# Kernel optimization log

Hardware: AMD Instinct MI355X
Metric: run time of the kernel (lower is better)

## Reference

```python
import jax, jax.numpy as jnp
import numpy as np


def setup_inputs() -> dict:
    key = jax.random.key(0)
    kq, kk, kv = jax.random.split(key, 3)
    B, S, H, D = 2, 2048, 16, 64
    q = jax.random.normal(kq, (B, S, H, D), dtype=jnp.float32)
    k = jax.random.normal(kk, (B, S, H, D), dtype=jnp.float32)
    v = jax.random.normal(kv, (B, S, H, D), dtype=jnp.float32)
    # additive key padding mask, [B,1,1,K]; 0 = unmasked, -inf = masked
    key_padding_mask = jnp.zeros((B, 1, 1, S), dtype=jnp.float32)
    return {"q": q, "k": k, "v": v, "key_padding_mask": key_padding_mask}


def reference(q, k, v, key_padding_mask):
    # q,k,v: [B, S, H, D]; key_padding_mask: [B,1,1,K] additive
    head_dim = q.shape[-1]
    softmax_scale = 1.0 / np.sqrt(head_dim).astype(np.float32)
    # [B, H, Q, K] logits with additive mask
    logits = jnp.einsum('bqhd,bkhd->bhqk', q, k) * softmax_scale + key_padding_mask
    attn = jax.nn.softmax(logits, axis=-1)
    # dropout p=0.0 -> identity in eval mode
    out = jnp.einsum('bhqk,bkhd->bqhd', attn, v)
    return out
```

## Files before the change

kernel.cpp:

```cpp
#include <hip/hip_runtime.h>
#include <hip/hip_bf16.h>


typedef __attribute__((ext_vector_type(8))) short bf16x8;
typedef __attribute__((ext_vector_type(4))) short bf16x4;
typedef __attribute__((ext_vector_type(4))) float f32x4;

#define B_ 2
#define S_ 2048
#define H_ 16
#define D_ 64
#define BQ 128
#define BK 64
#define NT (S_ / BK)
#define ROWSZ (H_ * D_)

#define LOG2E  1.44269504088896340736f
#define SCALE2 (0.125f * LOG2E)

__device__ __forceinline__ unsigned pack2(float a, float b) {
    union { __hip_bfloat162 h; unsigned u; } x;
    x.h = __float22bfloat162_rn(make_float2(a, b));
    return x.u;
}

__device__ __forceinline__ float fexp2(float x) {
#if __has_builtin(__builtin_amdgcn_exp2f)
    return __builtin_amdgcn_exp2f(x);
#else
    return __expf(x * 0.69314718055994531f);
#endif
}

__device__ __forceinline__ f32x4 mfma16(bf16x4 a, bf16x4 b, f32x4 c) {
#if __has_builtin(__builtin_amdgcn_mfma_f32_16x16x16bf16_1k)
    return __builtin_amdgcn_mfma_f32_16x16x16bf16_1k(a, b, c, 0, 0, 0);
#else
    bf16x8 a8 = {a[0], a[1], a[2], a[3], 0, 0, 0, 0};
    bf16x8 b8 = {b[0], b[1], b[2], b[3], 0, 0, 0, 0};
    return __builtin_amdgcn_mfma_f32_16x16x32_bf16(a8, b8, c, 0, 0, 0);
#endif
}

__global__ __launch_bounds__(512, 4)
void fattn_kernel(const float* __restrict__ qg,
                  const float* __restrict__ kg,
                  const float* __restrict__ vg,
                  const float* __restrict__ maskg,
                  float* __restrict__ outg)
{
    __shared__ __attribute__((aligned(16))) ushort Ks[2][4096];
    __shared__ __attribute__((aligned(16))) ushort Vt[2][4096];
    __shared__ __attribute__((aligned(16))) float  Em[S_];

    const int qt = blockIdx.x, h = blockIdx.y, b = blockIdx.z;
    const int tid = threadIdx.x;
    const int w = tid >> 6, lane = tid & 63, g = lane >> 4, l15 = lane & 15;

    {
        float4 mv = *(const float4*)(maskg + (size_t)b * S_ + tid * 4);
        *(float4*)&Em[tid * 4] = make_float4(mv.x * LOG2E, mv.y * LOG2E,
                                             mv.z * LOG2E, mv.w * LOG2E);
    }

    const int qrow = qt * BQ + w * 16 + l15;
    const float* qp = qg + (size_t)(b * S_ + qrow) * ROWSZ + h * D_;
    bf16x8 qf[2];
#pragma unroll
    for (int half = 0; half < 2; ++half) {
        float4 f0 = *(const float4*)(qp + half * 32 + g * 8);
        float4 f1 = *(const float4*)(qp + half * 32 + g * 8 + 4);
        union { bf16x8 v; uint4 u; } x;
        x.u = make_uint4(pack2(f0.x * SCALE2, f0.y * SCALE2),
                         pack2(f0.z * SCALE2, f0.w * SCALE2),
                         pack2(f1.x * SCALE2, f1.y * SCALE2),
                         pack2(f1.z * SCALE2, f1.w * SCALE2));
        qf[half] = x.v;
    }

    const int skey = tid >> 4;
    const int sd   = (tid & 15) * 4;
    const int kw0 = (skey >> 4) * 1024
                  + ((sd >> 3) + ((skey >> 3) & 1) * 8) * 64
                  + (((skey & 7) ^ (sd >> 3)) << 3) + (sd & 7);
    const int kw1 = kw0 + 2048;
    const int vwA = ((w >> 1) * 4 + (lane >> 4)) * 256
                  + ((2 * w) & 3) * 64 + (lane & 15) * 4;
    const int vwB = vwA + 64;

    const size_t kvbase = (size_t)b * S_ * ROWSZ + h * D_;

    float4 kpre0, kpre1;
    float  vpre[8];
    auto prefetch = [&](int kt) {
        const float* kb = kg + kvbase + (size_t)kt * BK * ROWSZ;
        kpre0 = *(const float4*)(kb + (size_t)skey * ROWSZ + sd);
        kpre1 = *(const float4*)(kb + (size_t)(skey + 32) * ROWSZ + sd);
        const float* vb = vg + kvbase + (size_t)kt * BK * ROWSZ + lane;
#pragma unroll
        for (int i = 0; i < 8; ++i) vpre[i] = vb[(size_t)(w * 8 + i) * ROWSZ];
    };
    auto stage = [&](int buf) {
        *(uint2*)&Ks[buf][kw0] =
            make_uint2(pack2(kpre0.x, kpre0.y), pack2(kpre0.z, kpre0.w));
        *(uint2*)&Ks[buf][kw1] =
            make_uint2(pack2(kpre1.x, kpre1.y), pack2(kpre1.z, kpre1.w));
        *(uint2*)&Vt[buf][vwA] =
            make_uint2(pack2(vpre[0], vpre[1]), pack2(vpre[2], vpre[3]));
        *(uint2*)&Vt[buf][vwB] =
            make_uint2(pack2(vpre[4], vpre[5]), pack2(vpre[6], vpre[7]));
    };

    float l_r = 0.0f;
    f32x4 o_acc[4];
#pragma unroll
    for (int t = 0; t < 4; ++t) o_acc[t] = (f32x4){0.f, 0.f, 0.f, 0.f};

    prefetch(0);
    stage(0);
    __syncthreads();

    const int krd0 = (g + (l15 >> 3) * 8) * 64 + (((l15 & 7) ^ g) << 3);
    const int krd1 = (g + 4 + (l15 >> 3) * 8) * 64 + (((l15 & 7) ^ (g + 4)) << 3);
    const int vrd = g * 64 + l15 * 4;

    for (int kt = 0; kt < NT; ++kt) {
        const int cur = kt & 1;
        if (kt + 1 < NT) prefetch(kt + 1);

        const ushort* ks = Ks[cur];
        float sv[4][4];
#pragma unroll
        for (int t = 0; t < 4; ++t) {
            f32x4 acc = *(const f32x4*)&Em[kt * BK + t * 16 + g * 4];
            bf16x8 kf0 = *(const bf16x8*)&ks[t * 1024 + krd0];
            bf16x8 kf1 = *(const bf16x8*)&ks[t * 1024 + krd1];
            acc = __builtin_amdgcn_mfma_f32_16x16x32_bf16(kf0, qf[0], acc, 0, 0, 0);
            acc = __builtin_amdgcn_mfma_f32_16x16x32_bf16(kf1, qf[1], acc, 0, 0, 0);
            sv[t][0] = acc[0]; sv[t][1] = acc[1]; sv[t][2] = acc[2]; sv[t][3] = acc[3];
        }

        float rs = 0.f;
#pragma unroll
        for (int t = 0; t < 4; ++t)
#pragma unroll
            for (int r = 0; r < 4; ++r) {
                float p = fexp2(sv[t][r]);
                sv[t][r] = p;
                rs += p;
            }
        l_r += rs;

        bf16x4 pf[4];
#pragma unroll
        for (int c = 0; c < 4; ++c) {
            union { bf16x4 v; uint2 u; } x;
            x.u = make_uint2(pack2(sv[c][0], sv[c][1]), pack2(sv[c][2], sv[c][3]));
            pf[c] = x.v;
        }

        const ushort* vt = Vt[cur];
#pragma unroll
        for (int c = 0; c < 4; ++c)
#pragma unroll
            for (int t2 = 0; t2 < 4; ++t2) {
                bf16x4 vf = *(const bf16x4*)&vt[(c * 4 + t2) * 256 + vrd];
                o_acc[t2] = mfma16(vf, pf[c], o_acc[t2]);
            }

        if (kt + 1 < NT) stage(cur ^ 1);
        __syncthreads();
    }

    l_r += __shfl_xor(l_r, 16);
    l_r += __shfl_xor(l_r, 32);
    const float inv = 1.0f / l_r;
    float* op = outg + (size_t)(b * S_ + qrow) * ROWSZ + h * D_;
#pragma unroll
    for (int t2 = 0; t2 < 4; ++t2)
#pragma unroll
        for (int r = 0; r < 4; ++r)
            op[t2 * 16 + g * 4 + r] = o_acc[t2][r] * inv;
}

extern "C" void kernel_launch(void* const* d_in, const int* in_sizes, int n_in,
                              void* d_out, int out_size, void* d_ws, size_t ws_size,
                              hipStream_t stream) {
    dim3 grid(S_ / BQ, H_, B_);
    fattn_kernel<<<grid, dim3(512), 0, stream>>>(
        (const float*)d_in[0], (const float*)d_in[1], (const float*)d_in[2],
        (const float*)d_in[3], (float*)d_out);
}
```

Baseline: 144.9 us.

## Split key sequence across two blocks and combine partial attention outputs

The attention kernel now splits the key/value sequence into two halves, each handled by its own block. Each block writes unnormalized partial outputs and row sums to workspace, and a second combine kernel adds them and normalizes. The goal is to double the number of blocks, raise occupancy and give the GPU more parallelism on a grid that was only 512 blocks. The exp/pack step is also folded into the QK loop. The cost is an extra kernel launch and substantial workspace write and read traffic; the original kernel is kept as a fallback when no workspace is provided.

New measurement: 170.2 us. 17.5% more time.

```diff
diff --git a/kernel.cpp b/kernel.cpp
--- a/kernel.cpp
+++ b/kernel.cpp
@@ -12,8 +12,13 @@
 #define D_ 64
 #define BQ 128
 #define BK 64
+#define QT_ (S_ / BQ)
+#define NSP 2
 #define NT (S_ / BK)
+#define NTH (NT / NSP)
 #define ROWSZ (H_ * D_)
+#define NREG (B_ * H_ * QT_ * NSP)
+#define REGSZ (512 * 16)
 
 #define LOG2E  1.44269504088896340736f
 #define SCALE2 (0.125f * LOG2E)
@@ -42,23 +47,26 @@
 #endif
 }
 
-__global__ __launch_bounds__(512, 4)
-void fattn_kernel(const float* __restrict__ qg,
-                  const float* __restrict__ kg,
-                  const float* __restrict__ vg,
-                  const float* __restrict__ maskg,
-                  float* __restrict__ outg)
+__global__ __launch_bounds__(512, 8)
+void fattn_split(const float* __restrict__ qg,
+                 const float* __restrict__ kg,
+                 const float* __restrict__ vg,
+                 const float* __restrict__ maskg,
+                 float* __restrict__ wso,
+                 float* __restrict__ wsl)
 {
     __shared__ __attribute__((aligned(16))) ushort Ks[2][4096];
     __shared__ __attribute__((aligned(16))) ushort Vt[2][4096];
-    __shared__ __attribute__((aligned(16))) float  Em[S_];
-
-    const int qt = blockIdx.x, h = blockIdx.y, b = blockIdx.z;
+    __shared__ __attribute__((aligned(16))) float  Em[S_ / NSP];
+
+    const int qt = blockIdx.x & 15, sp = blockIdx.x >> 4;
+    const int h = blockIdx.y, b = blockIdx.z;
     const int tid = threadIdx.x;
     const int w = tid >> 6, lane = tid & 63, g = lane >> 4, l15 = lane & 15;
 
-    {
-        float4 mv = *(const float4*)(maskg + (size_t)b * S_ + tid * 4);
+    if (tid < 256) {
+        float4 mv = *(const float4*)(maskg + (size_t)b * S_
+                                     + sp * (S_ / NSP) + tid * 4);
         *(float4*)&Em[tid * 4] = make_float4(mv.x * LOG2E, mv.y * LOG2E,
                                              mv.z * LOG2E, mv.w * LOG2E);
     }
@@ -88,15 +96,18 @@
                   + ((2 * w) & 3) * 64 + (lane & 15) * 4;
     const int vwB = vwA + 64;
 
-    const size_t kvbase = (size_t)b * S_ * ROWSZ + h * D_;
+    const size_t kvbase = (size_t)b * S_ * ROWSZ + h * D_
+                        + (size_t)sp * (S_ / NSP) * ROWSZ;
+    const float* kgs = kg + kvbase;
+    const float* vgs = vg + kvbase;
 
     float4 kpre0, kpre1;
     float  vpre[8];
-    auto prefetch = [&](int kt) {
-        const float* kb = kg + kvbase + (size_t)kt * BK * ROWSZ;
+    auto prefetch = [&](int ktl) {
+        const float* kb = kgs + (size_t)ktl * BK * ROWSZ;
         kpre0 = *(const float4*)(kb + (size_t)skey * ROWSZ + sd);
         kpre1 = *(const float4*)(kb + (size_t)(skey + 32) * ROWSZ + sd);
-        const float* vb = vg + kvbase + (size_t)kt * BK * ROWSZ + lane;
+        const float* vb = vgs + (size_t)ktl * BK * ROWSZ + lane;
 #pragma unroll
         for (int i = 0; i < 8; ++i) vpre[i] = vb[(size_t)(w * 8 + i) * ROWSZ];
     };
@@ -124,6 +135,162 @@
     const int krd1 = (g + 4 + (l15 >> 3) * 8) * 64 + (((l15 & 7) ^ (g + 4)) << 3);
     const int vrd = g * 64 + l15 * 4;
 
+    for (int ktl = 0; ktl < NTH; ++ktl) {
+        const int cur = ktl & 1;
+        if (ktl + 1 < NTH) prefetch(ktl + 1);
+
+        const ushort* ks = Ks[cur];
+        bf16x4 pf[4];
+        float rs = 0.f;
+#pragma unroll
+        for (int t = 0; t < 4; ++t) {
+            f32x4 acc = *(const f32x4*)&Em[ktl * BK + t * 16 + g * 4];
+            bf16x8 kf0 = *(const bf16x8*)&ks[t * 1024 + krd0];
+            bf16x8 kf1 = *(const bf16x8*)&ks[t * 1024 + krd1];
+            acc = __builtin_amdgcn_mfma_f32_16x16x32_bf16(kf0, qf[0], acc, 0, 0, 0);
+            acc = __builtin_amdgcn_mfma_f32_16x16x32_bf16(kf1, qf[1], acc, 0, 0, 0);
+            float p0 = fexp2(acc[0]), p1 = fexp2(acc[1]);
+            float p2 = fexp2(acc[2]), p3 = fexp2(acc[3]);
+            rs += (p0 + p1) + (p2 + p3);
+            union { bf16x4 v; uint2 u; } x;
+            x.u = make_uint2(pack2(p0, p1), pack2(p2, p3));
+            pf[t] = x.v;
+        }
+        l_r += rs;
+
+        const ushort* vt = Vt[cur];
+#pragma unroll
+        for (int c = 0; c < 4; ++c)
+#pragma unroll
+            for (int t2 = 0; t2 < 4; ++t2) {
+                bf16x4 vf = *(const bf16x4*)&vt[(c * 4 + t2) * 256 + vrd];
+                o_acc[t2] = mfma16(vf, pf[c], o_acc[t2]);
+            }
+
+        if (ktl + 1 < NTH) stage(cur ^ 1);
+        __syncthreads();
+    }
+
+    l_r += __shfl_xor(l_r, 16);
+    l_r += __shfl_xor(l_r, 32);
+
+    const int region = ((b * H_ + h) * QT_ + qt) * NSP + sp;
+    float* po = wso + (size_t)region * REGSZ + tid * 16;
+#pragma unroll
+    for (int t2 = 0; t2 < 4; ++t2) *(f32x4*)(po + t2 * 4) = o_acc[t2];
+    wsl[(size_t)region * 512 + tid] = l_r;
+}
+
+__global__ __launch_bounds__(512, 8)
+void fattn_combine(const float* __restrict__ wso,
+                   const float* __restrict__ wsl,
+                   float* __restrict__ outg)
+{
+    const int qt = blockIdx.x, h = blockIdx.y, b = blockIdx.z;
+    const int tid = threadIdx.x;
+    const int w = tid >> 6, lane = tid & 63, g = lane >> 4, l15 = lane & 15;
+
+    const int bhq = (b * H_ + h) * QT_ + qt;
+    const float* p0 = wso + (size_t)(bhq * NSP + 0) * REGSZ + tid * 16;
+    const float* p1 = wso + (size_t)(bhq * NSP + 1) * REGSZ + tid * 16;
+    const float  l  = wsl[(size_t)(bhq * NSP + 0) * 512 + tid]
+                    + wsl[(size_t)(bhq * NSP + 1) * 512 + tid];
+    const float inv = 1.0f / l;
+
+    const int qrow = qt * BQ + w * 16 + l15;
+    float* op = outg + (size_t)(b * S_ + qrow) * ROWSZ + h * D_;
+#pragma unroll
+    for (int t2 = 0; t2 < 4; ++t2) {
+        f32x4 a = *(const f32x4*)(p0 + t2 * 4);
+        f32x4 c = *(const f32x4*)(p1 + t2 * 4);
+#pragma unroll
+        for (int r = 0; r < 4; ++r)
+            op[t2 * 16 + g * 4 + r] = (a[r] + c[r]) * inv;
+    }
+}
+
+__global__ __launch_bounds__(512, 4)
+void fattn_kernel(const float* __restrict__ qg,
+                  const float* __restrict__ kg,
+                  const float* __restrict__ vg,
+                  const float* __restrict__ maskg,
+                  float* __restrict__ outg)
+{
+    __shared__ __attribute__((aligned(16))) ushort Ks[2][4096];
+    __shared__ __attribute__((aligned(16))) ushort Vt[2][4096];
+    __shared__ __attribute__((aligned(16))) float  Em[S_];
+
+    const int qt = blockIdx.x, h = blockIdx.y, b = blockIdx.z;
+    const int tid = threadIdx.x;
+    const int w = tid >> 6, lane = tid & 63, g = lane >> 4, l15 = lane & 15;
+
+    {
+        float4 mv = *(const float4*)(maskg + (size_t)b * S_ + tid * 4);
+        *(float4*)&Em[tid * 4] = make_float4(mv.x * LOG2E, mv.y * LOG2E,
+                                             mv.z * LOG2E, mv.w * LOG2E);
+    }
+
+    const int qrow = qt * BQ + w * 16 + l15;
+    const float* qp = qg + (size_t)(b * S_ + qrow) * ROWSZ + h * D_;
+    bf16x8 qf[2];
+#pragma unroll
+    for (int half = 0; half < 2; ++half) {
+        float4 f0 = *(const float4*)(qp + half * 32 + g * 8);
+        float4 f1 = *(const float4*)(qp + half * 32 + g * 8 + 4);
+        union { bf16x8 v; uint4 u; } x;
+        x.u = make_uint4(pack2(f0.x * SCALE2, f0.y * SCALE2),
+                         pack2(f0.z * SCALE2, f0.w * SCALE2),
+                         pack2(f1.x * SCALE2, f1.y * SCALE2),
+                         pack2(f1.z * SCALE2, f1.w * SCALE2));
+        qf[half] = x.v;
+    }
+
+    const int skey = tid >> 4;
+    const int sd   = (tid & 15) * 4;
+    const int kw0 = (skey >> 4) * 1024
+                  + ((sd >> 3) + ((skey >> 3) & 1) * 8) * 64
+                  + (((skey & 7) ^ (sd >> 3)) << 3) + (sd & 7);
+    const int kw1 = kw0 + 2048;
+    const int vwA = ((w >> 1) * 4 + (lane >> 4)) * 256
+                  + ((2 * w) & 3) * 64 + (lane & 15) * 4;
+    const int vwB = vwA + 64;
+
+    const size_t kvbase = (size_t)b * S_ * ROWSZ + h * D_;
+
+    float4 kpre0, kpre1;
+    float  vpre[8];
+    auto prefetch = [&](int kt) {
+        const float* kb = kg + kvbase + (size_t)kt * BK * ROWSZ;
+        kpre0 = *(const float4*)(kb + (size_t)skey * ROWSZ + sd);
+        kpre1 = *(const float4*)(kb + (size_t)(skey + 32) * ROWSZ + sd);
+        const float* vb = vg + kvbase + (size_t)kt * BK * ROWSZ + lane;
+#pragma unroll
+        for (int i = 0; i < 8; ++i) vpre[i] = vb[(size_t)(w * 8 + i) * ROWSZ];
+    };
+    auto stage = [&](int buf) {
+        *(uint2*)&Ks[buf][kw0] =
+            make_uint2(pack2(kpre0.x, kpre0.y), pack2(kpre0.z, kpre0.w));
+        *(uint2*)&Ks[buf][kw1] =
+            make_uint2(pack2(kpre1.x, kpre1.y), pack2(kpre1.z, kpre1.w));
+        *(uint2*)&Vt[buf][vwA] =
+            make_uint2(pack2(vpre[0], vpre[1]), pack2(vpre[2], vpre[3]));
+        *(uint2*)&Vt[buf][vwB] =
+            make_uint2(pack2(vpre[4], vpre[5]), pack2(vpre[6], vpre[7]));
+    };
+
+    float l_r = 0.0f;
+    f32x4 o_acc[4];
+#pragma unroll
+    for (int t = 0; t < 4; ++t) o_acc[t] = (f32x4){0.f, 0.f, 0.f, 0.f};
+
+    prefetch(0);
+    stage(0);
+    __syncthreads();
+
+    const int krd0 = (g + (l15 >> 3) * 8) * 64 + (((l15 & 7) ^ g) << 3);
+    const int krd1 = (g + 4 + (l15 >> 3) * 8) * 64 + (((l15 & 7) ^ (g + 4)) << 3);
+    const int vrd = g * 64 + l15 * 4;
+
     for (int kt = 0; kt < NT; ++kt) {
         const int cur = kt & 1;
         if (kt + 1 < NT) prefetch(kt + 1);
@@ -186,8 +353,22 @@
 extern "C" void kernel_launch(void* const* d_in, const int* in_sizes, int n_in,
                               void* d_out, int out_size, void* d_ws, size_t ws_size,
                               hipStream_t stream) {
-    dim3 grid(S_ / BQ, H_, B_);
-    fattn_kernel<<<grid, dim3(512), 0, stream>>>(
-        (const float*)d_in[0], (const float*)d_in[1], (const float*)d_in[2],
-        (const float*)d_in[3], (float*)d_out);
-}
+    const size_t O_BYTES = (size_t)NREG * REGSZ * 4;
+    const size_t L_BYTES = (size_t)NREG * 512 * 4;
+    const size_t NEED = O_BYTES + L_BYTES;
+    if (d_ws != nullptr && ws_size >= NEED) {
+        float* wso = (float*)d_ws;
+        float* wsl = (float*)((char*)d_ws + O_BYTES);
+        dim3 grid1(QT_ * NSP, H_, B_);
+        fattn_split<<<grid1, dim3(512), 0, stream>>>(
+            (const float*)d_in[0], (const float*)d_in[1], (const float*)d_in[2],
+            (const float*)d_in[3], wso, wsl);
+        dim3 grid2(QT_, H_, B_);
+        fattn_combine<<<grid2, dim3(512), 0, stream>>>(wso, wsl, (float*)d_out);
+    } else {
+        dim3 grid(QT_, H_, B_);
+        fattn_kernel<<<grid, dim3(512), 0, stream>>>(
+            (const float*)d_in[0], (const float*)d_in[1], (const float*)d_in[2],
+            (const float*)d_in[3], (float*)d_out);
+    }
+}
```
